# Kernel tuning notes

Hardware: AMD Instinct MI355X
Metric: run time of the kernel (lower is better)

The kernel has to match this reference:

```python
import jax, jax.numpy as jnp
import numpy as np

N_NODES = 200000
N_EDGES = 1600000
N_GRAPHS = 10000
IN_F = 74
HID = 128
OUT_F = 128
DEPTH = 3


def setup_inputs() -> dict:
    key = jax.random.key(0)
    ks = jax.random.split(key, 16)
    x = jax.random.normal(ks[0], (N_NODES, IN_F), dtype=jnp.float32)
    src = jax.random.randint(ks[1], (N_EDGES,), 0, N_NODES, dtype=jnp.int32)
    dst = jax.random.randint(ks[2], (N_EDGES,), 0, N_NODES, dtype=jnp.int32)
    graph_ids = jnp.sort(jax.random.randint(ks[3], (N_NODES,), 0, N_GRAPHS, dtype=jnp.int32))
    s = 1.0 / np.sqrt(HID)
    w_in = jax.random.normal(ks[4], (IN_F, HID), dtype=jnp.float32) / np.sqrt(IN_F)
    b_in = jnp.zeros((HID,), dtype=jnp.float32)
    gw = jax.random.normal(ks[5], (DEPTH, HID, HID), dtype=jnp.float32) * s
    gb = jnp.zeros((DEPTH, HID), dtype=jnp.float32)
    w_out = jax.random.normal(ks[6], (HID, HID), dtype=jnp.float32) * s
    b_out = jnp.zeros((HID,), dtype=jnp.float32)
    w_ff = jax.random.normal(ks[7], (HID, OUT_F), dtype=jnp.float32) * s
    b_ff = jnp.zeros((OUT_F,), dtype=jnp.float32)
    return {"x": x, "src": src, "dst": dst, "graph_ids": graph_ids,
            "w_in": w_in, "b_in": b_in, "gw": gw, "gb": gb,
            "w_out": w_out, "b_out": b_out, "w_ff": w_ff, "b_ff": b_ff}


def _graph_conv(h, src, dst, W, b, n_nodes):
    # DGL GraphConv, norm='both': D_out^{-1/2} gather -> scatter-add -> D_in^{-1/2}, then linear.
    ones = jnp.ones((src.shape[0],), dtype=h.dtype)
    deg_out = jax.ops.segment_sum(ones, src, num_segments=n_nodes)
    deg_in = jax.ops.segment_sum(ones, dst, num_segments=n_nodes)
    norm_src = jax.lax.rsqrt(jnp.maximum(deg_out, 1.0))  # [N]
    norm_dst = jax.lax.rsqrt(jnp.maximum(deg_in, 1.0))   # [N]
    hs = h * norm_src[:, None]
    agg = jax.ops.segment_sum(hs[src], dst, num_segments=n_nodes)  # SpMM
    agg = agg * norm_dst[:, None]
    return agg @ W + b


def reference(x, src, dst, graph_ids, w_in, b_in, gw, gb, w_out, b_out, w_ff, b_ff):
    silu = jax.nn.silu
    h = silu(x @ w_in + b_in)                       # embedding_in [N, HID]
    for i in range(DEPTH):
        h = silu(_graph_conv(h, src, dst, gw[i], gb[i], N_NODES))
    h = silu(h @ w_out + b_out)                     # embedding_out
    pooled = jax.ops.segment_sum(h, graph_ids, num_segments=N_GRAPHS)  # sum_nodes readout
    return pooled @ w_ff + b_ff                     # [G, OUT_F]
```

## Files before the change

kernel.cpp:

```cpp
#include <hip/hip_runtime.h>
#include <math.h>

#define N_NODES  200000
#define N_EDGES  1600000
#define N_GRAPHS 10000
#define IN_F     74
#define HID      128
#define DEPTH    3

#define NBUCK 391
#define G1    512
#define CHUNK 3125
#define NTOT  (NBUCK * G1)

typedef __attribute__((ext_vector_type(8))) short short8;
typedef __attribute__((ext_vector_type(8))) unsigned short ushort8v;
typedef __attribute__((ext_vector_type(4))) float floatx4;

__device__ __forceinline__ float silu_f(float x) {
    return x / (1.0f + __expf(-x));
}

__device__ __forceinline__ unsigned short f2bf(float f) {
    union { float f; unsigned int u; } v; v.f = f;
    unsigned int r = (v.u + 0x7fff + ((v.u >> 16) & 1)) >> 16;
    return (unsigned short)r;
}

__device__ __forceinline__ float bf2f(unsigned short u) {
    union { unsigned int u; float f; } v; v.u = ((unsigned int)u) << 16;
    return v.f;
}


__global__ void count_kernel(const int* __restrict__ src, const int* __restrict__ dst,
                             int* __restrict__ cnt_d, int* __restrict__ cnt_s) {
    __shared__ int hd[NBUCK], hs[NBUCK];
    int t = threadIdx.x, b = blockIdx.x;
    for (int i = t; i < NBUCK; i += 256) { hd[i] = 0; hs[i] = 0; }
    __syncthreads();
    int e0 = b * CHUNK;
    for (int i = t; i < CHUNK; i += 256) {
        int e = e0 + i;
        atomicAdd(&hd[dst[e] >> 9], 1);
        atomicAdd(&hs[src[e] >> 9], 1);
    }
    __syncthreads();
    for (int i = t; i < NBUCK; i += 256) {
        cnt_d[i * G1 + b] = hd[i];
        cnt_s[i * G1 + b] = hs[i];
    }
}

__global__ void gscan1(const int* __restrict__ in, int* __restrict__ out,
                       int* __restrict__ bsums, int n) {
    __shared__ int a[256], b2[256];
    int t = threadIdx.x;
    int i = blockIdx.x * 256 + t;
    a[t] = (i < n) ? in[i] : 0;
    __syncthreads();
    int* s = a; int* d = b2;
    #pragma unroll
    for (int off = 1; off < 256; off <<= 1) {
        int v = s[t];
        if (t >= off) v += s[t - off];
        d[t] = v;
        __syncthreads();
        int* tmp = s; s = d; d = tmp;
    }
    if (i < n) out[i] = (t ? s[t - 1] : 0);
    if (t == 255) bsums[blockIdx.x] = s[255];
}

__global__ void gscan2(int* __restrict__ bsums, int nb) {
    __shared__ int a[1024], b[1024];
    int t = threadIdx.x;
    a[t] = (t < nb) ? bsums[t] : 0;
    __syncthreads();
    int* s = a; int* d = b;
    for (int off = 1; off < 1024; off <<= 1) {
        int v = s[t];
        if (t >= off) v += s[t - off];
        d[t] = v;
        __syncthreads();
        int* tmp = s; s = d; d = tmp;
    }
    if (t < nb) bsums[t] = s[t];
}

__global__ void gscan3(int* __restrict__ out, const int* __restrict__ bsums, int n) {
    int i = blockIdx.x * 256 + threadIdx.x;
    if (i < n && blockIdx.x > 0) out[i] += bsums[blockIdx.x - 1];
}

__global__ void scatter_kernel(const int* __restrict__ src, const int* __restrict__ dst,
                               const int* __restrict__ offs_d, const int* __restrict__ offs_s,
                               int2* __restrict__ ebuf, int* __restrict__ sbuf) {
    __shared__ int cd[NBUCK], cs[NBUCK];
    int t = threadIdx.x, b = blockIdx.x;
    for (int i = t; i < NBUCK; i += 256) {
        cd[i] = offs_d[i * G1 + b];
        cs[i] = offs_s[i * G1 + b];
    }
    __syncthreads();
    int e0 = b * CHUNK;
    for (int i = t; i < CHUNK; i += 256) {
        int e = e0 + i;
        int d = dst[e], s = src[e];
        int pd = atomicAdd(&cd[d >> 9], 1);
        int2 p; p.x = d; p.y = s;
        ebuf[pd] = p;
        int ps = atomicAdd(&cs[s >> 9], 1);
        sbuf[ps] = s;
    }
}

__global__ __launch_bounds__(512)
void csr_kernel(const int2* __restrict__ ebuf, const int* __restrict__ offs_d,
                int* __restrict__ row_off, int* __restrict__ esrc,
                float* __restrict__ norm_dst) {
    __shared__ int deg[512];
    __shared__ int sa[512], sb[512];
    int k = blockIdx.x, t = threadIdx.x;
    int base = k << 9;
    int estart = offs_d[k * G1];
    int eend = (k + 1 < NBUCK) ? offs_d[(k + 1) * G1] : N_EDGES;
    deg[t] = 0;
    __syncthreads();
    for (int e = estart + t; e < eend; e += 512)
        atomicAdd(&deg[ebuf[e].x - base], 1);
    __syncthreads();
    sa[t] = deg[t];
    __syncthreads();
    int* ps = sa; int* pd = sb;
    #pragma unroll
    for (int off = 1; off < 512; off <<= 1) {
        int v = ps[t];
        if (t >= off) v += ps[t - off];
        pd[t] = v;
        __syncthreads();
        int* tmp = ps; ps = pd; pd = tmp;
    }
    int excl = t ? ps[t - 1] : 0;
    int n = base + t;
    if (n <= N_NODES) row_off[n] = estart + excl;
    if (n < N_NODES)  norm_dst[n] = rsqrtf(fmaxf((float)deg[t], 1.0f));
    __syncthreads();
    pd[t] = estart + excl;
    __syncthreads();
    for (int e = estart + t; e < eend; e += 512) {
        int2 ed = ebuf[e];
        int pos = atomicAdd(&pd[ed.x - base], 1);
        esrc[pos] = ed.y;
    }
}

__global__ __launch_bounds__(512)
void degsrc_kernel(const int* __restrict__ sbuf, const int* __restrict__ offs_s,
                   float* __restrict__ norm_src) {
    __shared__ int deg[512];
    int k = blockIdx.x, t = threadIdx.x;
    int base = k << 9;
    int estart = offs_s[k * G1];
    int eend = (k + 1 < NBUCK) ? offs_s[(k + 1) * G1] : N_EDGES;
    deg[t] = 0;
    __syncthreads();
    for (int e = estart + t; e < eend; e += 512)
        atomicAdd(&deg[sbuf[e] - base], 1);
    __syncthreads();
    int n = base + t;
    if (n < N_NODES) norm_src[n] = rsqrtf(fmaxf((float)deg[t], 1.0f));
}

__global__ void wprep_kernel(const float* __restrict__ w_in, const float* __restrict__ gw,
                             const float* __restrict__ w_out,
                             unsigned short* __restrict__ wtin,
                             unsigned short* __restrict__ wtg,
                             unsigned short* __restrict__ wtout)
{
    int i = blockIdx.x * 256 + threadIdx.x;
    if (i < 128 * 96) {
        int n = i / 96, k = i - n * 96;
        wtin[i] = (k < IN_F) ? f2bf(w_in[k * 128 + n]) : (unsigned short)0;
    } else if (i < 128 * 96 + 3 * 128 * 128) {
        int j = i - 128 * 96;
        int layer = j / 16384, r = j - layer * 16384;
        int n = r >> 7, k = r & 127;
        wtg[j] = f2bf(gw[((size_t)layer * 128 + k) * 128 + n]);
    } else if (i < 128 * 96 + 3 * 128 * 128 + 128 * 128) {
        int j = i - (128 * 96 + 3 * 128 * 128);
        int n = j >> 7, k = j & 127;
        wtout[j] = f2bf(w_out[k * 128 + n]);
    }
}

template<bool SCALE_NORM>
__launch_bounds__(256)
__global__ void fused_conv(const unsigned short* __restrict__ h,
                           const int* __restrict__ esrc, const int* __restrict__ row_off,
                           const float* __restrict__ norm_dst,
                           const unsigned short* __restrict__ WT,
                           const float* __restrict__ bias, const float* __restrict__ norm_src,
                           unsigned short* __restrict__ out) {
    __shared__ unsigned short lds_a[64 * 136];
    const int t = threadIdx.x;
    const int rowbase = blockIdx.x * 64;
    const int grp = t >> 4;
    const int lane16 = t & 15;

    #pragma unroll
    for (int g = 0; g < 4; ++g) {
        int r = g * 16 + grp;
        int node = rowbase + r;
        int beg = row_off[node], end = row_off[node + 1];
        float acc[8];
        #pragma unroll
        for (int q = 0; q < 8; ++q) acc[q] = 0.0f;
        int j = beg;
        for (; j + 3 < end; j += 4) {
            int s0 = esrc[j], s1 = esrc[j + 1], s2 = esrc[j + 2], s3 = esrc[j + 3];
            ushort8v v0 = *(const ushort8v*)(h + (size_t)s0 * HID + lane16 * 8);
            ushort8v v1 = *(const ushort8v*)(h + (size_t)s1 * HID + lane16 * 8);
            ushort8v v2 = *(const ushort8v*)(h + (size_t)s2 * HID + lane16 * 8);
            ushort8v v3 = *(const ushort8v*)(h + (size_t)s3 * HID + lane16 * 8);
            #pragma unroll
            for (int q = 0; q < 8; ++q)
                acc[q] += (bf2f(v0[q]) + bf2f(v1[q])) + (bf2f(v2[q]) + bf2f(v3[q]));
        }
        for (; j < end; ++j) {
            int s0 = esrc[j];
            ushort8v v0 = *(const ushort8v*)(h + (size_t)s0 * HID + lane16 * 8);
            #pragma unroll
            for (int q = 0; q < 8; ++q)
                acc[q] += bf2f(v0[q]);
        }
        float nd = norm_dst[node];
        ushort8v o;
        #pragma unroll
        for (int q = 0; q < 8; ++q) o[q] = f2bf(acc[q] * nd);
        *(ushort8v*)&lds_a[r * 136 + lane16 * 8] = o;
    }

    const int lane = t & 63;
    const int w  = t >> 6;
    const int wr = w & 1;
    const int wc = w >> 1;
    const int l15 = lane & 15, quad = lane >> 4;

    short8 bfrag[4][4];
    #pragma unroll
    for (int ks = 0; ks < 4; ++ks)
        #pragma unroll
        for (int tn = 0; tn < 4; ++tn) {
            int n = wc * 64 + tn * 16 + l15;
            bfrag[ks][tn] = *(const short8*)(WT + (size_t)n * 128 + ks * 32 + quad * 8);
        }

    floatx4 acc[4][2];
    #pragma unroll
    for (int tn = 0; tn < 4; ++tn)
        #pragma unroll
        for (int rt = 0; rt < 2; ++rt)
            acc[tn][rt] = (floatx4){0.f, 0.f, 0.f, 0.f};

    __syncthreads();

    #pragma unroll
    for (int ks = 0; ks < 4; ++ks) {
        short8 af[2];
        #pragma unroll
        for (int rt = 0; rt < 2; ++rt) {
            int m = wr * 32 + rt * 16 + l15;
            af[rt] = *(const short8*)&lds_a[m * 136 + ks * 32 + quad * 8];
        }
        #pragma unroll
        for (int tn = 0; tn < 4; ++tn)
            #pragma unroll
            for (int rt = 0; rt < 2; ++rt)
                acc[tn][rt] = __builtin_amdgcn_mfma_f32_16x16x32_bf16(
                    af[rt], bfrag[ks][tn], acc[tn][rt], 0, 0, 0);
    }

    __syncthreads();
    #pragma unroll
    for (int tn = 0; tn < 4; ++tn) {
        int col = wc * 64 + tn * 16 + l15;
        float b = bias[col];
        #pragma unroll
        for (int rt = 0; rt < 2; ++rt) {
            #pragma unroll
            for (int r = 0; r < 4; ++r) {
                int row = wr * 32 + rt * 16 + quad * 4 + r;
                float v = silu_f(acc[tn][rt][r] + b);
                if (SCALE_NORM) v *= norm_src[rowbase + row];
                lds_a[row * 136 + col] = f2bf(v);
            }
        }
    }
    __syncthreads();
    #pragma unroll
    for (int j = 0; j < 4; ++j) {
        int e = j * 256 + t;
        int r = e >> 4;
        int c = (e & 15) * 8;
        *(ushort8v*)(out + (size_t)(rowbase + r) * 128 + c) = *(const ushort8v*)&lds_a[r * 136 + c];
    }
}

template<int KP, bool A_BF16, bool SCALE_NORM>
__launch_bounds__(256)
__global__ void mfma_gemm(const void* __restrict__ in_, const unsigned short* __restrict__ WT,
                          const float* __restrict__ bias, const float* __restrict__ norm_src,
                          unsigned short* __restrict__ out, int nrows) {
    constexpr int KSTEPS = KP / 32;
    __shared__ unsigned short lds_a[64 * 136];
    const int t = threadIdx.x;
    const int rowbase = blockIdx.x * 64;

    if constexpr (A_BF16) {
        const unsigned short* in = (const unsigned short*)in_;
        #pragma unroll
        for (int j = 0; j < 4; ++j) {
            int e = j * 256 + t;
            int r = e >> 4;
            int c = (e & 15) * 8;
            ushort8v u = *(const ushort8v*)(in + (size_t)(rowbase + r) * KP + c);
            *(ushort8v*)&lds_a[r * 136 + c] = u;
        }
    } else {
        const float* in = (const float*)in_;
        for (int i = t; i < 64 * 37; i += 256) {
            int r = i / 37, kk = i - r * 37;
            float2 v = *(const float2*)(in + (size_t)(rowbase + r) * IN_F + kk * 2);
            lds_a[r * 136 + kk * 2]     = f2bf(v.x);
            lds_a[r * 136 + kk * 2 + 1] = f2bf(v.y);
        }
        for (int i = t; i < 64 * 22; i += 256) {
            int r = i / 22, kk = 74 + (i - r * 22);
            lds_a[r * 136 + kk] = 0;
        }
    }

    const int lane = t & 63;
    const int w  = t >> 6;
    const int wr = w & 1;
    const int wc = w >> 1;
    const int l15 = lane & 15, quad = lane >> 4;

    short8 bfrag[KSTEPS][4];
    #pragma unroll
    for (int ks = 0; ks < KSTEPS; ++ks)
        #pragma unroll
        for (int tn = 0; tn < 4; ++tn) {
            int n = wc * 64 + tn * 16 + l15;
            bfrag[ks][tn] = *(const short8*)(WT + (size_t)n * KP + ks * 32 + quad * 8);
        }

    floatx4 acc[4][2];
    #pragma unroll
    for (int tn = 0; tn < 4; ++tn)
        #pragma unroll
        for (int rt = 0; rt < 2; ++rt)
            acc[tn][rt] = (floatx4){0.f, 0.f, 0.f, 0.f};

    __syncthreads();

    #pragma unroll
    for (int ks = 0; ks < KSTEPS; ++ks) {
        short8 af[2];
        #pragma unroll
        for (int rt = 0; rt < 2; ++rt) {
            int m = wr * 32 + rt * 16 + l15;
            af[rt] = *(const short8*)&lds_a[m * 136 + ks * 32 + quad * 8];
        }
        #pragma unroll
        for (int tn = 0; tn < 4; ++tn)
            #pragma unroll
            for (int rt = 0; rt < 2; ++rt)
                acc[tn][rt] = __builtin_amdgcn_mfma_f32_16x16x32_bf16(
                    af[rt], bfrag[ks][tn], acc[tn][rt], 0, 0, 0);
    }

    __syncthreads();
    #pragma unroll
    for (int tn = 0; tn < 4; ++tn) {
        int col = wc * 64 + tn * 16 + l15;
        float b = bias[col];
        #pragma unroll
        for (int rt = 0; rt < 2; ++rt) {
            #pragma unroll
            for (int r = 0; r < 4; ++r) {
                int row = wr * 32 + rt * 16 + quad * 4 + r;
                float v = silu_f(acc[tn][rt][r] + b);
                if (SCALE_NORM) v *= norm_src[rowbase + row];
                lds_a[row * 136 + col] = f2bf(v);
            }
        }
    }
    __syncthreads();
    #pragma unroll
    for (int j = 0; j < 4; ++j) {
        int e = j * 256 + t;
        int r = e >> 4;
        int c = (e & 15) * 8;
        *(ushort8v*)(out + (size_t)(rowbase + r) * 128 + c) = *(const ushort8v*)&lds_a[r * 136 + c];
    }
}

template<int K, bool DO_SILU>
__launch_bounds__(256)
__global__ void gemm_kernel(const float* __restrict__ in, const float* __restrict__ W,
                            const float* __restrict__ bias, float* __restrict__ out, int nrows) {
    __shared__ float wl[64 * HID];
    __shared__ float xl[32 * K];
    int t = threadIdx.x;
    int row0 = blockIdx.x * 32;

    for (int i = t; i < 32 * K; i += 256) {
        int r = i / K, k = i - r * K;
        int gr = row0 + r;
        xl[i] = (gr < nrows) ? in[(size_t)gr * K + k] : 0.0f;
    }

    int col = t & (HID - 1);
    int rg  = t >> 7;
    float acc[16];
    #pragma unroll
    for (int rr = 0; rr < 16; ++rr) acc[rr] = 0.0f;

    for (int c = 0; c < K; c += 64) {
        int kc = (K - c < 64) ? (K - c) : 64;
        __syncthreads();
        for (int i = t; i < kc * HID; i += 256) wl[i] = W[(size_t)c * HID + i];
        __syncthreads();
        for (int kk = 0; kk < kc; ++kk) {
            float w = wl[kk * HID + col];
            int k = c + kk;
            #pragma unroll
            for (int rr = 0; rr < 16; ++rr)
                acc[rr] += xl[(rg * 16 + rr) * K + k] * w;
        }
    }

    float b = bias[col];
    #pragma unroll
    for (int rr = 0; rr < 16; ++rr) {
        int r = row0 + rg * 16 + rr;
        if (r < nrows) {
            float v = acc[rr] + b;
            if (DO_SILU) v = silu_f(v);
            out[(size_t)r * HID + col] = v;
        }
    }
}

__device__ __forceinline__ int lower_bound_gid(const int* __restrict__ gid, int val) {
    int lo = 0, hi = N_NODES;
    while (lo < hi) {
        int mid = (lo + hi) >> 1;
        if (gid[mid] < val) lo = mid + 1; else hi = mid;
    }
    return lo;
}

__global__ void pool_kernel(const unsigned short* __restrict__ h, const int* __restrict__ gid,
                            float* __restrict__ pooled) {
    int g = blockIdx.x;
    int t = threadIdx.x;
    int beg = lower_bound_gid(gid, g);
    int end = lower_bound_gid(gid, g + 1);
    float s = 0.0f;
    for (int n = beg; n < end; ++n)
        s += bf2f(h[(size_t)n * HID + t]);
    pooled[(size_t)g * HID + t] = s;
}

extern "C" void kernel_launch(void* const* d_in, const int* in_sizes, int n_in,
                              void* d_out, int out_size, void* d_ws, size_t ws_size,
                              hipStream_t stream) {
    const float* x     = (const float*)d_in[0];
    const int*   src   = (const int*)  d_in[1];
    const int*   dst   = (const int*)  d_in[2];
    const int*   gid   = (const int*)  d_in[3];
    const float* w_in  = (const float*)d_in[4];
    const float* b_in  = (const float*)d_in[5];
    const float* gw    = (const float*)d_in[6];
    const float* gb    = (const float*)d_in[7];
    const float* w_out = (const float*)d_in[8];
    const float* b_out = (const float*)d_in[9];
    const float* w_ff  = (const float*)d_in[10];
    const float* b_ff  = (const float*)d_in[11];
    float* out = (float*)d_out;

    char* w = (char*)d_ws;
    size_t off = 0;
    auto alloc = [&](size_t bytes) { void* p = w + off; off += (bytes + 255) & ~(size_t)255; return p; };
    unsigned short* hb0 = (unsigned short*)alloc((size_t)N_NODES * HID * 2);
    unsigned short* hb1 = (unsigned short*)alloc((size_t)N_NODES * HID * 2);
    float* norm_src = (float*)alloc((size_t)N_NODES * 4);
    float* norm_dst = (float*)alloc((size_t)N_NODES * 4);
    int*   row_off  = (int*)  alloc((size_t)(N_NODES + 1) * 4);
    int*   esrc     = (int*)  alloc((size_t)N_EDGES * 4);
    int2*  ebuf     = (int2*) alloc((size_t)N_EDGES * 8);
    int*   sbuf     = (int*)  alloc((size_t)N_EDGES * 4);
    int*   cnt_d    = (int*)  alloc((size_t)NTOT * 4);
    int*   cnt_s    = (int*)  alloc((size_t)NTOT * 4);
    int*   offs_d   = (int*)  alloc((size_t)NTOT * 4);
    int*   offs_s   = (int*)  alloc((size_t)NTOT * 4);
    int*   bsums    = (int*)  alloc(1024 * 4);
    float* pooled   = (float*)alloc((size_t)N_GRAPHS * HID * 4);
    unsigned short* wtin  = (unsigned short*)alloc(128 * 96 * 2);
    unsigned short* wtg   = (unsigned short*)alloc(3 * 128 * 128 * 2);
    unsigned short* wtout = (unsigned short*)alloc(128 * 128 * 2);

    const int NB_SCAN = NTOT / 256;

    count_kernel<<<G1, 256, 0, stream>>>(src, dst, cnt_d, cnt_s);
    gscan1<<<NB_SCAN, 256, 0, stream>>>(cnt_d, offs_d, bsums, NTOT);
    gscan2<<<1, 1024, 0, stream>>>(bsums, NB_SCAN);
    gscan3<<<NB_SCAN, 256, 0, stream>>>(offs_d, bsums, NTOT);
    gscan1<<<NB_SCAN, 256, 0, stream>>>(cnt_s, offs_s, bsums, NTOT);
    gscan2<<<1, 1024, 0, stream>>>(bsums, NB_SCAN);
    gscan3<<<NB_SCAN, 256, 0, stream>>>(offs_s, bsums, NTOT);
    scatter_kernel<<<G1, 256, 0, stream>>>(src, dst, offs_d, offs_s, ebuf, sbuf);
    csr_kernel<<<NBUCK, 512, 0, stream>>>(ebuf, offs_d, row_off, esrc, norm_dst);
    degsrc_kernel<<<NBUCK, 512, 0, stream>>>(sbuf, offs_s, norm_src);

    wprep_kernel<<<(128 * 96 + 4 * 128 * 128 + 255) / 256, 256, 0, stream>>>(
        w_in, gw, w_out, wtin, wtg, wtout);

    const int NB_M = N_NODES / 64;

    mfma_gemm<96, false, true><<<NB_M, 256, 0, stream>>>(
        x, wtin, b_in, norm_src, hb0, N_NODES);

    fused_conv<true><<<NB_M, 256, 0, stream>>>(
        hb0, esrc, row_off, norm_dst, wtg + 0 * HID * HID, gb + 0 * HID, norm_src, hb1);
    fused_conv<true><<<NB_M, 256, 0, stream>>>(
        hb1, esrc, row_off, norm_dst, wtg + 1 * HID * HID, gb + 1 * HID, norm_src, hb0);
    fused_conv<false><<<NB_M, 256, 0, stream>>>(
        hb0, esrc, row_off, norm_dst, wtg + 2 * HID * HID, gb + 2 * HID, norm_src, hb1);

    mfma_gemm<128, true, false><<<NB_M, 256, 0, stream>>>(
        hb1, wtout, b_out, norm_src, hb0, N_NODES);

    pool_kernel<<<N_GRAPHS, HID, 0, stream>>>(hb0, gid, pooled);

    gemm_kernel<HID, false><<<(N_GRAPHS + 31) / 32, 256, 0, stream>>>(pooled, w_ff, b_ff, out, N_GRAPHS);
}
```

Baseline: 701.0 us.

## Fuse output projection into last conv, stage weights in LDS, widen gather unroll

Folds the embedding_out GEMM into the third graph-conv kernel as a second MFMA pass, which removes one full read and write of the node feature matrix. Weight tiles are now staged cooperatively in LDS instead of being loaded per wave into registers, which lowers register pressure and raises occupancy at the cost of more LDS per block. The neighbor gather is unrolled to 8 edges for more memory-level parallelism. The pool kernel now handles four graphs per block and reads two bf16 values per lane.

```diff
diff --git a/kernel.cpp b/kernel.cpp
--- a/kernel.cpp
+++ b/kernel.cpp
@@ -194,19 +194,29 @@
     }
 }
 
-template<bool SCALE_NORM>
+template<bool SCALE_NORM, bool SECOND>
 __launch_bounds__(256)
 __global__ void fused_conv(const unsigned short* __restrict__ h,
                            const int* __restrict__ esrc, const int* __restrict__ row_off,
                            const float* __restrict__ norm_dst,
                            const unsigned short* __restrict__ WT,
                            const float* __restrict__ bias, const float* __restrict__ norm_src,
+                           const unsigned short* __restrict__ WT2,
+                           const float* __restrict__ bias2,
                            unsigned short* __restrict__ out) {
     __shared__ unsigned short lds_a[64 * 136];
+    __shared__ unsigned short lds_b[128 * 136];
     const int t = threadIdx.x;
     const int rowbase = blockIdx.x * 64;
     const int grp = t >> 4;
     const int lane16 = t & 15;
+
+    #pragma unroll
+    for (int j = 0; j < 8; ++j) {
+        int slot = j * 256 + t;
+        int n = slot >> 4, k = (slot & 15) * 8;
+        *(ushort8v*)&lds_b[n * 136 + k] = *(const ushort8v*)(WT + n * 128 + k);
+    }
 
     #pragma unroll
     for (int g = 0; g < 4; ++g) {
@@ -217,19 +227,27 @@
         #pragma unroll
         for (int q = 0; q < 8; ++q) acc[q] = 0.0f;
         int j = beg;
+        for (; j + 7 < end; j += 8) {
+            ushort8v v[8];
+            #pragma unroll
+            for (int u = 0; u < 8; ++u)
+                v[u] = *(const ushort8v*)(h + (size_t)esrc[j + u] * HID + lane16 * 8);
+            #pragma unroll
+            for (int q = 0; q < 8; ++q)
+                acc[q] += ((bf2f(v[0][q]) + bf2f(v[1][q])) + (bf2f(v[2][q]) + bf2f(v[3][q])))
+                        + ((bf2f(v[4][q]) + bf2f(v[5][q])) + (bf2f(v[6][q]) + bf2f(v[7][q])));
+        }
         for (; j + 3 < end; j += 4) {
-            int s0 = esrc[j], s1 = esrc[j + 1], s2 = esrc[j + 2], s3 = esrc[j + 3];
-            ushort8v v0 = *(const ushort8v*)(h + (size_t)s0 * HID + lane16 * 8);
-            ushort8v v1 = *(const ushort8v*)(h + (size_t)s1 * HID + lane16 * 8);
-            ushort8v v2 = *(const ushort8v*)(h + (size_t)s2 * HID + lane16 * 8);
-            ushort8v v3 = *(const ushort8v*)(h + (size_t)s3 * HID + lane16 * 8);
+            ushort8v v[4];
+            #pragma unroll
+            for (int u = 0; u < 4; ++u)
+                v[u] = *(const ushort8v*)(h + (size_t)esrc[j + u] * HID + lane16 * 8);
             #pragma unroll
             for (int q = 0; q < 8; ++q)
-                acc[q] += (bf2f(v0[q]) + bf2f(v1[q])) + (bf2f(v2[q]) + bf2f(v3[q]));
+                acc[q] += (bf2f(v[0][q]) + bf2f(v[1][q])) + (bf2f(v[2][q]) + bf2f(v[3][q]));
         }
         for (; j < end; ++j) {
-            int s0 = esrc[j];
-            ushort8v v0 = *(const ushort8v*)(h + (size_t)s0 * HID + lane16 * 8);
+            ushort8v v0 = *(const ushort8v*)(h + (size_t)esrc[j] * HID + lane16 * 8);
             #pragma unroll
             for (int q = 0; q < 8; ++q)
                 acc[q] += bf2f(v0[q]);
@@ -247,15 +265,6 @@
     const int wc = w >> 1;
     const int l15 = lane & 15, quad = lane >> 4;
 
-    short8 bfrag[4][4];
-    #pragma unroll
-    for (int ks = 0; ks < 4; ++ks)
-        #pragma unroll
-        for (int tn = 0; tn < 4; ++tn) {
-            int n = wc * 64 + tn * 16 + l15;
-            bfrag[ks][tn] = *(const short8*)(WT + (size_t)n * 128 + ks * 32 + quad * 8);
-        }
-
     floatx4 acc[4][2];
     #pragma unroll
     for (int tn = 0; tn < 4; ++tn)
@@ -267,21 +276,24 @@
 
     #pragma unroll
     for (int ks = 0; ks < 4; ++ks) {
+        short8 bk[4];
+        #pragma unroll
+        for (int tn = 0; tn < 4; ++tn)
+            bk[tn] = *(const short8*)&lds_b[(wc * 64 + tn * 16 + l15) * 136 + ks * 32 + quad * 8];
         short8 af[2];
         #pragma unroll
-        for (int rt = 0; rt < 2; ++rt) {
-            int m = wr * 32 + rt * 16 + l15;
-            af[rt] = *(const short8*)&lds_a[m * 136 + ks * 32 + quad * 8];
-        }
+        for (int rt = 0; rt < 2; ++rt)
+            af[rt] = *(const short8*)&lds_a[(wr * 32 + rt * 16 + l15) * 136 + ks * 32 + quad * 8];
         #pragma unroll
         for (int tn = 0; tn < 4; ++tn)
             #pragma unroll
             for (int rt = 0; rt < 2; ++rt)
                 acc[tn][rt] = __builtin_amdgcn_mfma_f32_16x16x32_bf16(
-                    af[rt], bfrag[ks][tn], acc[tn][rt], 0, 0, 0);
-    }
-
-    __syncthreads();
+                    af[rt], bk[tn], acc[tn][rt], 0, 0, 0);
+    }
+
+    __syncthreads();
+
     #pragma unroll
     for (int tn = 0; tn < 4; ++tn) {
         int col = wc * 64 + tn * 16 + l15;
@@ -297,6 +309,55 @@
             }
         }
     }
+
+    if constexpr (SECOND) {
+        #pragma unroll
+        for (int j = 0; j < 8; ++j) {
+            int slot = j * 256 + t;
+            int n = slot >> 4, k = (slot & 15) * 8;
+            *(ushort8v*)&lds_b[n * 136 + k] = *(const ushort8v*)(WT2 + n * 128 + k);
+        }
+        #pragma unroll
+        for (int tn = 0; tn < 4; ++tn)
+            #pragma unroll
+            for (int rt = 0; rt < 2; ++rt)
+                acc[tn][rt] = (floatx4){0.f, 0.f, 0.f, 0.f};
+        __syncthreads();
+
+        #pragma unroll
+        for (int ks = 0; ks < 4; ++ks) {
+            short8 bk[4];
+            #pragma unroll
+            for (int tn = 0; tn < 4; ++tn)
+                bk[tn] = *(const short8*)&lds_b[(wc * 64 + tn * 16 + l15) * 136 + ks * 32 + quad * 8];
+            short8 af[2];
+            #pragma unroll
+            for (int rt = 0; rt < 2; ++rt)
+                af[rt] = *(const short8*)&lds_a[(wr * 32 + rt * 16 + l15) * 136 + ks * 32 + quad * 8];
+            #pragma unroll
+            for (int tn = 0; tn < 4; ++tn)
+                #pragma unroll
+                for (int rt = 0; rt < 2; ++rt)
+                    acc[tn][rt] = __builtin_amdgcn_mfma_f32_16x16x32_bf16(
+                        af[rt], bk[tn], acc[tn][rt], 0, 0, 0);
+        }
+
+        __syncthreads();
+        #pragma unroll
+        for (int tn = 0; tn < 4; ++tn) {
+            int col = wc * 64 + tn * 16 + l15;
+            float b = bias2[col];
+            #pragma unroll
+            for (int rt = 0; rt < 2; ++rt) {
+                #pragma unroll
+                for (int r = 0; r < 4; ++r) {
+                    int row = wr * 32 + rt * 16 + quad * 4 + r;
+                    lds_a[row * 136 + col] = f2bf(silu_f(acc[tn][rt][r] + b));
+                }
+            }
+        }
+    }
+
     __syncthreads();
     #pragma unroll
     for (int j = 0; j < 4; ++j) {
@@ -307,38 +368,32 @@
     }
 }
 
-template<int KP, bool A_BF16, bool SCALE_NORM>
 __launch_bounds__(256)
-__global__ void mfma_gemm(const void* __restrict__ in_, const unsigned short* __restrict__ WT,
-                          const float* __restrict__ bias, const float* __restrict__ norm_src,
-                          unsigned short* __restrict__ out, int nrows) {
-    constexpr int KSTEPS = KP / 32;
-    __shared__ unsigned short lds_a[64 * 136];
+__global__ void inproj_gemm(const float* __restrict__ in, const unsigned short* __restrict__ WT,
+                            const float* __restrict__ bias, const float* __restrict__ norm_src,
+                            unsigned short* __restrict__ out) {
+    constexpr int KP = 96, ASTR = 136, BSTR = 104;
+    __shared__ unsigned short lds_a[64 * ASTR];
+    __shared__ unsigned short lds_b[128 * BSTR];
     const int t = threadIdx.x;
     const int rowbase = blockIdx.x * 64;
 
-    if constexpr (A_BF16) {
-        const unsigned short* in = (const unsigned short*)in_;
-        #pragma unroll
-        for (int j = 0; j < 4; ++j) {
-            int e = j * 256 + t;
-            int r = e >> 4;
-            int c = (e & 15) * 8;
-            ushort8v u = *(const ushort8v*)(in + (size_t)(rowbase + r) * KP + c);
-            *(ushort8v*)&lds_a[r * 136 + c] = u;
-        }
-    } else {
-        const float* in = (const float*)in_;
-        for (int i = t; i < 64 * 37; i += 256) {
-            int r = i / 37, kk = i - r * 37;
-            float2 v = *(const float2*)(in + (size_t)(rowbase + r) * IN_F + kk * 2);
-            lds_a[r * 136 + kk * 2]     = f2bf(v.x);
-            lds_a[r * 136 + kk * 2 + 1] = f2bf(v.y);
-        }
-        for (int i = t; i < 64 * 22; i += 256) {
-            int r = i / 22, kk = 74 + (i - r * 22);
-            lds_a[r * 136 + kk] = 0;
-        }
+    #pragma unroll
+    for (int j = 0; j < 6; ++j) {
+        int slot = j * 256 + t;
+        int n = slot / 12, k = (slot - n * 12) * 8;
+        *(ushort8v*)&lds_b[n * BSTR + k] = *(const ushort8v*)(WT + n * KP + k);
+    }
+
+    for (int i = t; i < 64 * 37; i += 256) {
+        int r = i / 37, kk = (i - r * 37) * 2;
+        float2 v = *(const float2*)(in + (size_t)(rowbase + r) * IN_F + kk);
+        lds_a[r * ASTR + kk]     = f2bf(v.x);
+        lds_a[r * ASTR + kk + 1] = f2bf(v.y);
+    }
+    for (int i = t; i < 64 * 22; i += 256) {
+        int r = i / 22, kk = 74 + (i - r * 22);
+        lds_a[r * ASTR + kk] = 0;
     }
 
     const int lane = t & 63;
@@ -347,15 +402,6 @@
     const int wc = w >> 1;
     const int l15 = lane & 15, quad = lane >> 4;
 
-    short8 bfrag[KSTEPS][4];
-    #pragma unroll
-    for (int ks = 0; ks < KSTEPS; ++ks)
-        #pragma unroll
-        for (int tn = 0; tn < 4; ++tn) {
-            int n = wc * 64 + tn * 16 + l15;
-            bfrag[ks][tn] = *(const short8*)(WT + (size_t)n * KP + ks * 32 + quad * 8);
-        }
-
     floatx4 acc[4][2];
     #pragma unroll
     for (int tn = 0; tn < 4; ++tn)
@@ -366,19 +412,21 @@
     __syncthreads();
 
     #pragma unroll
-    for (int ks = 0; ks < KSTEPS; ++ks) {
+    for (int ks = 0; ks < 3; ++ks) {
+        short8 bk[4];
+        #pragma unroll
+        for (int tn = 0; tn < 4; ++tn)
+            bk[tn] = *(const short8*)&lds_b[(wc * 64 + tn * 16 + l15) * BSTR + ks * 32 + quad * 8];
         short8 af[2];
         #pragma unroll
-        for (int rt = 0; rt < 2; ++rt) {
-            int m = wr * 32 + rt * 16 + l15;
-            af[rt] = *(const short8*)&lds_a[m * 136 + ks * 32 + quad * 8];
-        }
+        for (int rt = 0; rt < 2; ++rt)
+            af[rt] = *(const short8*)&lds_a[(wr * 32 + rt * 16 + l15) * ASTR + ks * 32 + quad * 8];
         #pragma unroll
         for (int tn = 0; tn < 4; ++tn)
             #pragma unroll
             for (int rt = 0; rt < 2; ++rt)
                 acc[tn][rt] = __builtin_amdgcn_mfma_f32_16x16x32_bf16(
-                    af[rt], bfrag[ks][tn], acc[tn][rt], 0, 0, 0);
+                    af[rt], bk[tn], acc[tn][rt], 0, 0, 0);
     }
 
     __syncthreads();
@@ -391,9 +439,8 @@
             #pragma unroll
             for (int r = 0; r < 4; ++r) {
                 int row = wr * 32 + rt * 16 + quad * 4 + r;
-                float v = silu_f(acc[tn][rt][r] + b);
-                if (SCALE_NORM) v *= norm_src[rowbase + row];
-                lds_a[row * 136 + col] = f2bf(v);
+                float v = silu_f(acc[tn][rt][r] + b) * norm_src[rowbase + row];
+                lds_a[row * ASTR + col] = f2bf(v);
             }
         }
     }
@@ -403,7 +450,7 @@
         int e = j * 256 + t;
         int r = e >> 4;
         int c = (e & 15) * 8;
-        *(ushort8v*)(out + (size_t)(rowbase + r) * 128 + c) = *(const ushort8v*)&lds_a[r * 136 + c];
+        *(ushort8v*)(out + (size_t)(rowbase + r) * 128 + c) = *(const ushort8v*)&lds_a[r * ASTR + c];
     }
 }
 
@@ -465,14 +512,19 @@
 
 __global__ void pool_kernel(const unsigned short* __restrict__ h, const int* __restrict__ gid,
                             float* __restrict__ pooled) {
-    int g = blockIdx.x;
-    int t = threadIdx.x;
+    int g = blockIdx.x * 4 + (threadIdx.x >> 6);
+    int lane = threadIdx.x & 63;
     int beg = lower_bound_gid(gid, g);
     int end = lower_bound_gid(gid, g + 1);
-    float s = 0.0f;
-    for (int n = beg; n < end; ++n)
-        s += bf2f(h[(size_t)n * HID + t]);
-    pooled[(size_t)g * HID + t] = s;
+    float s0 = 0.0f, s1 = 0.0f;
+    const unsigned int* hp = (const unsigned int*)h;
+    for (int n = beg; n < end; ++n) {
+        unsigned int u = hp[(size_t)n * 64 + lane];
+        s0 += bf2f((unsigned short)(u & 0xffff));
+        s1 += bf2f((unsigned short)(u >> 16));
+    }
+    float2 o; o.x = s0; o.y = s1;
+    *(float2*)(pooled + (size_t)g * HID + lane * 2) = o;
 }
 
 extern "C" void kernel_launch(void* const* d_in, const int* in_sizes, int n_in,
@@ -531,20 +583,19 @@
 
     const int NB_M = N_NODES / 64;
 
-    mfma_gemm<96, false, true><<<NB_M, 256, 0, stream>>>(
-        x, wtin, b_in, norm_src, hb0, N_NODES);
-
-    fused_conv<true><<<NB_M, 256, 0, stream>>>(
-        hb0, esrc, row_off, norm_dst, wtg + 0 * HID * HID, gb + 0 * HID, norm_src, hb1);
-    fused_conv<true><<<NB_M, 256, 0, stream>>>(
-        hb1, esrc, row_off, norm_dst, wtg + 1 * HID * HID, gb + 1 * HID, norm_src, hb0);
-    fused_conv<false><<<NB_M, 256, 0, stream>>>(
-        hb0, esrc, row_off, norm_dst, wtg + 2 * HID * HID, gb + 2 * HID, norm_src, hb1);
-
-    mfma_gemm<128, true, false><<<NB_M, 256, 0, stream>>>(
-        hb1, wtout, b_out, norm_src, hb0, N_NODES);
-
-    pool_kernel<<<N_GRAPHS, HID, 0, stream>>>(hb0, gid, pooled);
+    inproj_gemm<<<NB_M, 256, 0, stream>>>(x, wtin, b_in, norm_src, hb0);
+
+    fused_conv<true,  false><<<NB_M, 256, 0, stream>>>(
+        hb0, esrc, row_off, norm_dst, wtg + 0 * HID * HID, gb + 0 * HID, norm_src,
+        (const unsigned short*)nullptr, (const float*)nullptr, hb1);
+    fused_conv<true,  false><<<NB_M, 256, 0, stream>>>(
+        hb1, esrc, row_off, norm_dst, wtg + 1 * HID * HID, gb + 1 * HID, norm_src,
+        (const unsigned short*)nullptr, (const float*)nullptr, hb0);
+    fused_conv<false, true><<<NB_M, 256, 0, stream>>>(
+        hb0, esrc, row_off, norm_dst, wtg + 2 * HID * HID, gb + 2 * HID, norm_src,
+        wtout, b_out, hb1);
+
+    pool_kernel<<<N_GRAPHS / 4, 256, 0, stream>>>(hb1, gid, pooled);
 
     gemm_kernel<HID, false><<<(N_GRAPHS + 31) / 32, 256, 0, stream>>>(pooled, w_ff, b_ff, out, N_GRAPHS);
 }
```

Result: faster. 618.2 us (-11.8%).
